# Performance work log

Measured on AMD Instinct MI355X. Metric: run time of the kernel, lower is better.

## Reference

```python
import jax, jax.numpy as jnp
import numpy as np

N_NODES = 50000
VOCAB = 2048
HID = 256
N_EDGES = 1600000


def setup_inputs() -> dict:
    key = jax.random.key(0)
    ks = jax.random.split(key, 7)
    context = jax.random.normal(ks[0], (N_NODES, VOCAB), dtype=jnp.float32)
    adj_row = jax.random.randint(ks[1], (N_EDGES,), 0, N_NODES, dtype=jnp.int64)
    adj_col = jax.random.randint(ks[2], (N_EDGES,), 0, N_NODES, dtype=jnp.int64)
    adj_val = jax.random.uniform(ks[3], (N_EDGES,), dtype=jnp.float32)
    # learned params
    context_weight = jax.random.normal(ks[4], (HID, VOCAB), dtype=jnp.float32) * 0.02
    out_w = jax.random.normal(ks[5], (VOCAB, HID), dtype=jnp.float32) * 0.02
    out_b = jnp.zeros((VOCAB,), dtype=jnp.float32)
    return {
        "context": context,
        "adj_row": adj_row,
        "adj_col": adj_col,
        "adj_val": adj_val,
        "context_weight": context_weight,
        "out_w": out_w,
        "out_b": out_b,
    }


def reference(context, adj_row, adj_col, adj_val, context_weight, out_w, out_b):
    # support = context @ context_weight.T : [N, hid]
    support = jnp.einsum('nv,hv->nh', context, context_weight)
    # spmm: out[r] += val * support[c]  (COO sparse-dense matmul)
    gathered = support[adj_col] * adj_val[:, None]          # [E, hid]
    agg = jax.ops.segment_sum(gathered, adj_row, num_segments=N_NODES)  # [N, hid]
    score = jax.nn.relu(agg)
    # out linear: hid -> vocab
    output = jnp.einsum('nh,vh->nv', score, out_w) + out_b  # [N, vocab]
    return output
```

## Files before the change

kernel.cpp:

```cpp
#include <hip/hip_runtime.h>
#include <hip/hip_bf16.h>

#define N_NODES 50000
#define VOCAB   2048
#define HID     256
#define N_EDGES 1600000

typedef __attribute__((ext_vector_type(8))) __bf16 bf16x8;
typedef __attribute__((ext_vector_type(4))) __bf16 bf16x4;
typedef __attribute__((ext_vector_type(4))) float  f32x4;

__device__ __forceinline__ void gl_lds16(const void* g, void* l) {
    __builtin_amdgcn_global_load_lds(
        (const __attribute__((address_space(1))) void*)g,
        (__attribute__((address_space(3))) void*)l, 16, 0, 0);
}

#define ZERO_NB 49
__global__ __launch_bounds__(256) void phase1(
    const float* __restrict__ w, __bf16* __restrict__ wb, int n4,
    int* __restrict__ cnt, int ncnt)
{
    int bid = blockIdx.x;
    if (bid < ZERO_NB) {
        const int base = bid * 1024 + threadIdx.x * 4;
        if (base + 3 < ncnt)      *(int4*)&cnt[base] = make_int4(0, 0, 0, 0);
        else                      for (int i = 0; i < 4; ++i)
                                      if (base + i < ncnt) cnt[base + i] = 0;
        return;
    }
    const int t = (bid - ZERO_NB) * 256 + threadIdx.x;
    if (t < n4) {
        const float4 v = ((const float4*)w)[t];
        bf16x4 p = { (__bf16)v.x, (__bf16)v.y, (__bf16)v.z, (__bf16)v.w };
        ((bf16x4*)wb)[t] = p;
    }
}

#define HIST_NB 96
#define CVTW_NB 64
__global__ __launch_bounds__(256) void phase2(
    const float*  __restrict__ Af,
    const __bf16* __restrict__ Bb,
    __bf16*       __restrict__ Cb,
    int M,
    const int*    __restrict__ arow, int* __restrict__ cnt, int E,
    const float*  __restrict__ w2,   __bf16* __restrict__ w2b, int n4w)
{
    const int tid = threadIdx.x;
    int bid = blockIdx.x;

    if (bid < HIST_NB) {
        const int stride = HIST_NB * 256;
        for (int e4 = bid * 256 + tid; e4 < E / 4; e4 += stride) {
            const int4 r = ((const int4*)arow)[e4];
            atomicAdd(&cnt[r.x], 1); atomicAdd(&cnt[r.y], 1);
            atomicAdd(&cnt[r.z], 1); atomicAdd(&cnt[r.w], 1);
        }
        return;
    }
    bid -= HIST_NB;
    if (bid < CVTW_NB) {
        const int stride = CVTW_NB * 256;
        for (int t = bid * 256 + tid; t < n4w; t += stride) {
            const float4 v = ((const float4*)w2)[t];
            bf16x4 p = { (__bf16)v.x, (__bf16)v.y, (__bf16)v.z, (__bf16)v.w };
            ((bf16x4*)w2b)[t] = p;
        }
        return;
    }
    bid -= CVTW_NB;

    constexpr int K = 2048, N = 256, BM = 64, BK = 32, nkt = K / BK;
    __shared__ float  sAf[3][BM * BK];
    __shared__ __bf16 sB [3][N  * BK];

    const int lane = tid & 63;
    const int wn   = tid >> 6;
    const int half = lane >> 4;
    const int r16  = lane & 15;
    const int m0   = bid * BM;

    f32x4 acc[4][4] = {};

    auto stage = [&](int kt, int b) {
        const int k0 = kt * BK;
        #pragma unroll
        for (int i = 0; i < 2; ++i) {
            const int s   = i * 256 + tid;
            const int row = s >> 3, c = s & 7;
            const int csw = c ^ (row & 7);
            int gr = m0 + row; if (gr >= M) gr = M - 1;
            gl_lds16(&Af[(size_t)gr * K + k0 + csw * 4], &sAf[b][s * 4]);
        }
        #pragma unroll
        for (int i = 0; i < 4; ++i) {
            const int s   = i * 256 + tid;
            const int row = s >> 2, c = s & 3;
            const int csw = c ^ (row & 3);
            gl_lds16(&Bb[(size_t)row * K + k0 + csw * 8], &sB[b][s * 8]);
        }
    };
    auto step = [&](int b) {
        bf16x8 bfr[4];
        #pragma unroll
        for (int n = 0; n < 4; ++n) {
            const int brow = wn * 64 + n * 16 + r16;
            bfr[n] = *(const bf16x8*)&sB[b][brow * 32 + (half ^ (brow & 3)) * 8];
        }
        #pragma unroll
        for (int m = 0; m < 4; ++m) {
            const int arw = m * 16 + r16;
            const int rx  = arw & 7;
            const f32x4 lo = *(const f32x4*)&sAf[b][arw * 32 + ((2 * half)     ^ rx) * 4];
            const f32x4 hi = *(const f32x4*)&sAf[b][arw * 32 + ((2 * half + 1) ^ rx) * 4];
            const bf16x8 af = { (__bf16)lo.x, (__bf16)lo.y, (__bf16)lo.z, (__bf16)lo.w,
                                (__bf16)hi.x, (__bf16)hi.y, (__bf16)hi.z, (__bf16)hi.w };
            #pragma unroll
            for (int n = 0; n < 4; ++n)
                acc[m][n] = __builtin_amdgcn_mfma_f32_16x16x32_bf16(
                                af, bfr[n], acc[m][n], 0, 0, 0);
        }
    };

    stage(0, 0);
    stage(1, 1);
    for (int t = 0; t < nkt; ++t) {
        if (t + 1 < nkt) asm volatile("s_waitcnt vmcnt(6)" ::: "memory");
        else             asm volatile("s_waitcnt vmcnt(0)" ::: "memory");
        __builtin_amdgcn_s_barrier();
        __builtin_amdgcn_sched_barrier(0);
        step(t % 3);
        if (t + 2 < nkt) stage(t + 2, (t + 2) % 3);
    }

    #pragma unroll
    for (int m = 0; m < 4; ++m) {
        #pragma unroll
        for (int j = 0; j < 4; ++j) {
            const int gr = m0 + m * 16 + half * 4 + j;
            if (gr >= M) continue;
            #pragma unroll
            for (int n = 0; n < 4; ++n) {
                const int gc = wn * 64 + n * 16 + r16;
                Cb[(size_t)gr * N + gc] = (__bf16)acc[m][n][j];
            }
        }
    }
}

#define SCAN_NB 49

__global__ __launch_bounds__(256) void scan1(
    const int* __restrict__ cnt, int* __restrict__ bsum, int n)
{
    __shared__ int red[256];
    const int base = blockIdx.x * 1024 + threadIdx.x * 4;
    int s = 0;
    #pragma unroll
    for (int i = 0; i < 4; ++i) { const int idx = base + i; if (idx < n) s += cnt[idx]; }
    red[threadIdx.x] = s;
    __syncthreads();
    for (int off = 128; off > 0; off >>= 1) {
        if (threadIdx.x < off) red[threadIdx.x] += red[threadIdx.x + off];
        __syncthreads();
    }
    if (threadIdx.x == 0) bsum[blockIdx.x] = red[0];
}

__global__ __launch_bounds__(256) void scan3m(
    const int* __restrict__ cnt, const int* __restrict__ bsum,
    int* __restrict__ ptr, int* __restrict__ cursor, int n, int E)
{
    __shared__ int hs[256];
    __shared__ int pre[256];
    const int tid = threadIdx.x;
    pre[tid] = (tid < blockIdx.x && tid < SCAN_NB) ? bsum[tid] : 0;
    __syncthreads();
    for (int off = 128; off > 0; off >>= 1) {
        if (tid < off) pre[tid] += pre[tid + off];
        __syncthreads();
    }
    const int bbase = pre[0];

    const int base = blockIdx.x * 1024 + tid * 4;
    int loc[4]; int s = 0;
    #pragma unroll
    for (int i = 0; i < 4; ++i) {
        const int idx = base + i;
        loc[i] = (idx < n) ? cnt[idx] : 0;
        s += loc[i];
    }
    hs[tid] = s;
    __syncthreads();
    for (int off = 1; off < 256; off <<= 1) {
        int v = (tid >= off) ? hs[tid - off] : 0;
        __syncthreads();
        hs[tid] += v;
        __syncthreads();
    }
    int run = bbase + ((tid == 0) ? 0 : hs[tid - 1]);
    #pragma unroll
    for (int i = 0; i < 4; ++i) {
        const int idx = base + i;
        if (idx < n) { ptr[idx] = run; cursor[idx] = run; }
        run += loc[i];
    }
    if (blockIdx.x == 0 && tid == 0) ptr[n] = E;
}

__global__ __launch_bounds__(256) void csr_fill(
    const int*   __restrict__ arow,
    const int*   __restrict__ acol,
    const float* __restrict__ aval,
    int*         __restrict__ cursor,
    int2*        __restrict__ cpair,
    int E)
{
    const int stride = gridDim.x * blockDim.x;
    for (int e4 = blockIdx.x * blockDim.x + threadIdx.x; e4 < E / 4; e4 += stride) {
        const int4   r = ((const int4*)arow)[e4];
        const int4   c = ((const int4*)acol)[e4];
        const float4 v = ((const float4*)aval)[e4];
        int p;
        p = atomicAdd(&cursor[r.x], 1); cpair[p] = make_int2(c.x, __float_as_int(v.x));
        p = atomicAdd(&cursor[r.y], 1); cpair[p] = make_int2(c.y, __float_as_int(v.y));
        p = atomicAdd(&cursor[r.z], 1); cpair[p] = make_int2(c.z, __float_as_int(v.z));
        p = atomicAdd(&cursor[r.w], 1); cpair[p] = make_int2(c.w, __float_as_int(v.w));
    }
}

__global__ __launch_bounds__(256) void spmm_gather(
    const int*    __restrict__ ptr,
    const int2*   __restrict__ cpair,
    const __bf16* __restrict__ support,
    __bf16*       __restrict__ agg,
    int n)
{
    const int tid  = threadIdx.x;
    const int lane = tid & 63;
    const int row  = blockIdx.x * 4 + (tid >> 6);
    if (row >= n) return;
    const int l32 = lane & 31, ep = lane >> 5;
    const int beg = ptr[row], end = ptr[row + 1];

    float a[8] = {0.f, 0.f, 0.f, 0.f, 0.f, 0.f, 0.f, 0.f};

    auto fma8 = [&](float v, const uint4& s) {
        a[0] += v * __uint_as_float(s.x << 16);
        a[1] += v * __uint_as_float(s.x & 0xFFFF0000u);
        a[2] += v * __uint_as_float(s.y << 16);
        a[3] += v * __uint_as_float(s.y & 0xFFFF0000u);
        a[4] += v * __uint_as_float(s.z << 16);
        a[5] += v * __uint_as_float(s.z & 0xFFFF0000u);
        a[6] += v * __uint_as_float(s.w << 16);
        a[7] += v * __uint_as_float(s.w & 0xFFFF0000u);
    };

    int i = beg;
    for (; i + 16 <= end; i += 16) {
        int2 p[8];
        #pragma unroll
        for (int u = 0; u < 8; ++u) p[u] = cpair[i + 2 * u + ep];
        uint4 s[8];
        #pragma unroll
        for (int u = 0; u < 8; ++u)
            s[u] = *(const uint4*)&support[(size_t)p[u].x * HID + l32 * 8];
        #pragma unroll
        for (int u = 0; u < 8; ++u) fma8(__int_as_float(p[u].y), s[u]);
    }
    for (; i + 2 <= end; i += 2) {
        const int2 p = cpair[i + ep];
        const uint4 s = *(const uint4*)&support[(size_t)p.x * HID + l32 * 8];
        fma8(__int_as_float(p.y), s);
    }
    if (i < end && ep == 0) {
        const int2 p = cpair[i];
        const uint4 s = *(const uint4*)&support[(size_t)p.x * HID + l32 * 8];
        fma8(__int_as_float(p.y), s);
    }

    #pragma unroll
    for (int k = 0; k < 8; ++k) a[k] += __shfl_xor(a[k], 32);

    if (ep == 0) {
        bf16x8 o = { (__bf16)fmaxf(a[0], 0.f), (__bf16)fmaxf(a[1], 0.f),
                     (__bf16)fmaxf(a[2], 0.f), (__bf16)fmaxf(a[3], 0.f),
                     (__bf16)fmaxf(a[4], 0.f), (__bf16)fmaxf(a[5], 0.f),
                     (__bf16)fmaxf(a[6], 0.f), (__bf16)fmaxf(a[7], 0.f) };
        *(bf16x8*)&agg[(size_t)row * HID + l32 * 8] = o;
    }
}

__global__ __launch_bounds__(256) void gemm2(
    const __bf16* __restrict__ Ab,
    const __bf16* __restrict__ Bb,
    const float*  __restrict__ bias,
    float*        __restrict__ C,
    int M)
{
    constexpr int K = 256, N = 2048, BM = 128, BN = 128, BK = 32;
    constexpr int NBY = N / BN, nkt = K / BK;
    __shared__ __bf16 sA[3][BM * BK];
    __shared__ __bf16 sB[3][BN * BK];

    const int tid  = threadIdx.x;
    const int lane = tid & 63;
    const int wid  = tid >> 6;
    const int wm   = wid >> 1;
    const int wn   = wid & 1;
    const int half = lane >> 4;
    const int r16  = lane & 15;

    const int nwg = gridDim.x, cpx = nwg >> 3;
    const int wg  = (blockIdx.x & 7) * cpx + (blockIdx.x >> 3);
    const int m0  = (wg / NBY) * BM;
    const int n0  = (wg % NBY) * BN;

    f32x4 acc[4][4] = {};

    auto stage = [&](int kt, int b) {
        const int k0 = kt * BK;
        #pragma unroll
        for (int i = 0; i < 2; ++i) {
            const int s   = i * 256 + tid;
            const int row = s >> 2, c = s & 3;
            const int csw = c ^ (row & 3);
            int gr = m0 + row; if (gr >= M) gr = M - 1;
            gl_lds16(&Ab[(size_t)gr * K + k0 + csw * 8], &sA[b][s * 8]);
        }
        #pragma unroll
        for (int i = 0; i < 2; ++i) {
            const int s   = i * 256 + tid;
            const int row = s >> 2, c = s & 3;
            const int csw = c ^ (row & 3);
            gl_lds16(&Bb[(size_t)(n0 + row) * K + k0 + csw * 8], &sB[b][s * 8]);
        }
    };
    auto step = [&](int b) {
        bf16x8 bfr[4];
        #pragma unroll
        for (int n = 0; n < 4; ++n) {
            const int brow = wn * 64 + n * 16 + r16;
            bfr[n] = *(const bf16x8*)&sB[b][brow * 32 + (half ^ (brow & 3)) * 8];
        }
        #pragma unroll
        for (int m = 0; m < 4; ++m) {
            const int arw = wm * 64 + m * 16 + r16;
            const bf16x8 af = *(const bf16x8*)&sA[b][arw * 32 + (half ^ (arw & 3)) * 8];
            #pragma unroll
            for (int n = 0; n < 4; ++n)
                acc[m][n] = __builtin_amdgcn_mfma_f32_16x16x32_bf16(
                                af, bfr[n], acc[m][n], 0, 0, 0);
        }
    };

    stage(0, 0);
    stage(1, 1);
    for (int t = 0; t < nkt; ++t) {
        if (t + 1 < nkt) asm volatile("s_waitcnt vmcnt(4)" ::: "memory");
        else             asm volatile("s_waitcnt vmcnt(0)" ::: "memory");
        __builtin_amdgcn_s_barrier();
        __builtin_amdgcn_sched_barrier(0);
        step(t % 3);
        if (t + 2 < nkt) stage(t + 2, (t + 2) % 3);
    }

    #pragma unroll
    for (int m = 0; m < 4; ++m) {
        #pragma unroll
        for (int j = 0; j < 4; ++j) {
            const int gr = m0 + wm * 64 + m * 16 + half * 4 + j;
            if (gr >= M) continue;
            #pragma unroll
            for (int n = 0; n < 4; ++n) {
                const int gc = n0 + wn * 64 + n * 16 + r16;
                __builtin_nontemporal_store(acc[m][n][j] + bias[gc],
                                            &C[(size_t)gr * N + gc]);
            }
        }
    }
}

extern "C" void kernel_launch(void* const* d_in, const int* in_sizes, int n_in,
                              void* d_out, int out_size, void* d_ws, size_t ws_size,
                              hipStream_t stream) {
    const float* context  = (const float*)d_in[0];
    const int*   adj_row  = (const int*)  d_in[1];
    const int*   adj_col  = (const int*)  d_in[2];
    const float* adj_val  = (const float*)d_in[3];
    const float* ctx_w    = (const float*)d_in[4];
    const float* out_w    = (const float*)d_in[5];
    const float* out_b    = (const float*)d_in[6];
    float*       out      = (float*)d_out;

    char* ws = (char*)d_ws;
    __bf16* support_b = (__bf16*)ws;  ws += (size_t)N_NODES * HID * 2;
    __bf16* agg_b     = (__bf16*)ws;  ws += (size_t)N_NODES * HID * 2;
    __bf16* ctxw_b    = (__bf16*)ws;  ws += (size_t)HID * VOCAB * 2;
    __bf16* outw_b    = (__bf16*)ws;  ws += (size_t)VOCAB * HID * 2;
    int*    csr_ptr   = (int*)ws;     ws += ((size_t)N_NODES + 16) * 4;
    int*    cnt       = (int*)ws;     ws += (size_t)N_NODES * 4;
    int*    cursor    = (int*)ws;     ws += (size_t)N_NODES * 4;
    int*    bsum      = (int*)ws;     ws += 320;
    int2*   cpair     = (int2*)ws;    ws += (size_t)N_EDGES * 8;

    constexpr int N4 = HID * VOCAB / 4;

    phase1<<<dim3(ZERO_NB + (N4 + 255) / 256), 256, 0, stream>>>(
        ctx_w, ctxw_b, N4, cnt, N_NODES);

    phase2<<<dim3(HIST_NB + CVTW_NB + (N_NODES + 63) / 64), 256, 0, stream>>>(
        context, ctxw_b, support_b, N_NODES,
        adj_row, cnt, N_EDGES,
        out_w, outw_b, N4);

    scan1<<<SCAN_NB, 256, 0, stream>>>(cnt, bsum, N_NODES);
    scan3m<<<SCAN_NB, 256, 0, stream>>>(cnt, bsum, csr_ptr, cursor, N_NODES, N_EDGES);

    csr_fill<<<512, 256, 0, stream>>>(
        adj_row, adj_col, adj_val, cursor, cpair, N_EDGES);

    spmm_gather<<<(N_NODES + 3) / 4, 256, 0, stream>>>(
        csr_ptr, cpair, support_b, agg_b, N_NODES);

    gemm2<<<dim3(((N_NODES + 127) / 128) * (VOCAB / 128)), 256, 0, stream>>>(
        agg_b, outw_b, out_b, out, N_NODES);
}
```

Baseline: 494.1 us.

## Pipeline SpMM row chunks with output GEMM tiles across fused launches

Splits the rows into three chunks and fuses the SpMM gather for chunk i+1 with the output GEMM for chunk i in one launch, so the gather-bound and MFMA-bound blocks share the GPU at the same time. This is meant to hide the SpMM latency and fill the tail of each phase. In exchange it adds launches, and the mixed kernels carry the GEMM's shared-memory footprint for SpMM blocks too, which may lower occupancy for the gather work.

After: 558.1 us. 13.0% more time.

```diff
diff --git a/kernel.cpp b/kernel.cpp
--- a/kernel.cpp
+++ b/kernel.cpp
@@ -230,17 +230,17 @@
     }
 }
 
-__global__ __launch_bounds__(256) void spmm_gather(
+__device__ __forceinline__ void spmm_rows(
+    int bid, int tid,
     const int*    __restrict__ ptr,
     const int2*   __restrict__ cpair,
     const __bf16* __restrict__ support,
     __bf16*       __restrict__ agg,
-    int n)
-{
-    const int tid  = threadIdx.x;
+    int rowLo, int rowHi)
+{
     const int lane = tid & 63;
-    const int row  = blockIdx.x * 4 + (tid >> 6);
-    if (row >= n) return;
+    const int row  = rowLo + bid * 4 + (tid >> 6);
+    if (row >= rowHi) return;
     const int l32 = lane & 31, ep = lane >> 5;
     const int beg = ptr[row], end = ptr[row + 1];
 
@@ -292,19 +292,19 @@
     }
 }
 
-__global__ __launch_bounds__(256) void gemm2(
+__device__ __forceinline__ void gemm2_tile(
+    int bid, int nBlocks, int tid,
     const __bf16* __restrict__ Ab,
     const __bf16* __restrict__ Bb,
     const float*  __restrict__ bias,
     float*        __restrict__ C,
-    int M)
+    int M, int tLo)
 {
     constexpr int K = 256, N = 2048, BM = 128, BN = 128, BK = 32;
     constexpr int NBY = N / BN, nkt = K / BK;
     __shared__ __bf16 sA[3][BM * BK];
     __shared__ __bf16 sB[3][BN * BK];
 
-    const int tid  = threadIdx.x;
     const int lane = tid & 63;
     const int wid  = tid >> 6;
     const int wm   = wid >> 1;
@@ -312,9 +312,9 @@
     const int half = lane >> 4;
     const int r16  = lane & 15;
 
-    const int nwg = gridDim.x, cpx = nwg >> 3;
-    const int wg  = (blockIdx.x & 7) * cpx + (blockIdx.x >> 3);
-    const int m0  = (wg / NBY) * BM;
+    const int cpx = nBlocks >> 3;
+    const int wg  = (bid & 7) * cpx + (bid >> 3);
+    const int m0  = (tLo + wg / NBY) * BM;
     const int n0  = (wg % NBY) * BN;
 
     f32x4 acc[4][4] = {};
@@ -380,6 +380,38 @@
             }
         }
     }
+}
+
+__global__ __launch_bounds__(256) void spmm_k(
+    const int* __restrict__ ptr, const int2* __restrict__ cpair,
+    const __bf16* __restrict__ support, __bf16* __restrict__ agg,
+    int rowLo, int rowHi)
+{
+    spmm_rows(blockIdx.x, threadIdx.x, ptr, cpair, support, agg, rowLo, rowHi);
+}
+
+__global__ __launch_bounds__(256) void gemm2_k(
+    const __bf16* __restrict__ Ab, const __bf16* __restrict__ Bb,
+    const float* __restrict__ bias, float* __restrict__ C,
+    int M, int tLo)
+{
+    gemm2_tile(blockIdx.x, gridDim.x, threadIdx.x, Ab, Bb, bias, C, M, tLo);
+}
+
+__global__ __launch_bounds__(256) void spmm_gemm2_k(
+    const int* __restrict__ ptr, const int2* __restrict__ cpair,
+    const __bf16* __restrict__ support, __bf16* __restrict__ agg,
+    int rowLo, int rowHi, int spmmNB,
+    const __bf16* __restrict__ Ab, const __bf16* __restrict__ Bb,
+    const float* __restrict__ bias, float* __restrict__ C,
+    int M, int tLo, int g2NB)
+{
+    const int bid = blockIdx.x;
+    if (bid < spmmNB) {
+        spmm_rows(bid, threadIdx.x, ptr, cpair, support, agg, rowLo, rowHi);
+        return;
+    }
+    gemm2_tile(bid - spmmNB, g2NB, threadIdx.x, Ab, Bb, bias, C, M, tLo);
 }
 
 extern "C" void kernel_launch(void* const* d_in, const int* in_sizes, int n_in,
@@ -421,9 +453,21 @@
     csr_fill<<<512, 256, 0, stream>>>(
         adj_row, adj_col, adj_val, cursor, cpair, N_EDGES);
 
-    spmm_gather<<<(N_NODES + 3) / 4, 256, 0, stream>>>(
-        csr_ptr, cpair, support_b, agg_b, N_NODES);
-
-    gemm2<<<dim3(((N_NODES + 127) / 128) * (VOCAB / 128)), 256, 0, stream>>>(
-        agg_b, outw_b, out_b, out, N_NODES);
-}
+    constexpr int T0 = 130, T1 = 130, T2 = 131;
+    constexpr int R1 = T0 * 128;
+    constexpr int R2 = (T0 + T1) * 128;
+    constexpr int S0 = (R1 + 3) / 4;
+    constexpr int S1 = (R2 - R1 + 3) / 4;
+    constexpr int S2 = (N_NODES - R2 + 3) / 4;
+    constexpr int G0 = T0 * 16, G1 = T1 * 16, G2 = T2 * 16;
+
+    spmm_k<<<S0, 256, 0, stream>>>(csr_ptr, cpair, support_b, agg_b, 0, R1);
+    spmm_gemm2_k<<<S1 + G0, 256, 0, stream>>>(
+        csr_ptr, cpair, support_b, agg_b, R1, R2, S1,
+        agg_b, outw_b, out_b, out, N_NODES, 0, G0);
+    spmm_gemm2_k<<<S2 + G1, 256, 0, stream>>>(
+        csr_ptr, cpair, support_b, agg_b, R2, N_NODES, S2,
+        agg_b, outw_b, out_b, out, N_NODES, T0, G1);
+    gemm2_k<<<G2, 256, 0, stream>>>(
+        agg_b, outw_b, out_b, out, N_NODES, T0 + T1);
+}
```

## Load GEMM1 B operand directly to registers and enlarge K tile with double buffering

Applied to the files above, without the earlier changes.

The first GEMM (context × weightᵀ) no longer stages the bf16 weight tile through LDS. Each wave now reads its B fragments straight from global memory into registers. The K tile grows from 32 to 128, and the A tile moves from triple-buffered to double-buffered LDS with a wider swizzle. The aim is to cut LDS traffic and barrier count per K step. The cost is a full vmcnt(0) wait each iteration, so prefetch depth is lower, and B loads from global may be less coalesced and add latency.

Result: no change. 491.1 us (median of 2 runs) (-0.6%).

```diff
diff --git a/kernel.cpp b/kernel.cpp
--- a/kernel.cpp
+++ b/kernel.cpp
@@ -71,9 +71,8 @@
     }
     bid -= CVTW_NB;
 
-    constexpr int K = 2048, N = 256, BM = 64, BK = 32, nkt = K / BK;
-    __shared__ float  sAf[3][BM * BK];
-    __shared__ __bf16 sB [3][N  * BK];
+    constexpr int K = 2048, N = 256, BM = 64, BK = 128, nkt = K / BK;
+    __shared__ float sAf[2][BM * BK];
 
     const int lane = tid & 63;
     const int wn   = tid >> 6;
@@ -86,52 +85,51 @@
     auto stage = [&](int kt, int b) {
         const int k0 = kt * BK;
         #pragma unroll
-        for (int i = 0; i < 2; ++i) {
+        for (int i = 0; i < 8; ++i) {
             const int s   = i * 256 + tid;
-            const int row = s >> 3, c = s & 7;
-            const int csw = c ^ (row & 7);
+            const int row = s >> 5, c = s & 31;
+            const int csw = (c & 24) | ((c & 7) ^ (row & 7));
             int gr = m0 + row; if (gr >= M) gr = M - 1;
-            gl_lds16(&Af[(size_t)gr * K + k0 + csw * 4], &sAf[b][s * 4]);
-        }
-        #pragma unroll
-        for (int i = 0; i < 4; ++i) {
-            const int s   = i * 256 + tid;
-            const int row = s >> 2, c = s & 3;
-            const int csw = c ^ (row & 3);
-            gl_lds16(&Bb[(size_t)row * K + k0 + csw * 8], &sB[b][s * 8]);
+            gl_lds16(&Af[(size_t)gr * K + k0 + csw * 4], &sAf[b][row * BK + c * 4]);
         }
     };
-    auto step = [&](int b) {
-        bf16x8 bfr[4];
-        #pragma unroll
-        for (int n = 0; n < 4; ++n) {
-            const int brow = wn * 64 + n * 16 + r16;
-            bfr[n] = *(const bf16x8*)&sB[b][brow * 32 + (half ^ (brow & 3)) * 8];
-        }
-        #pragma unroll
-        for (int m = 0; m < 4; ++m) {
-            const int arw = m * 16 + r16;
-            const int rx  = arw & 7;
-            const f32x4 lo = *(const f32x4*)&sAf[b][arw * 32 + ((2 * half)     ^ rx) * 4];
-            const f32x4 hi = *(const f32x4*)&sAf[b][arw * 32 + ((2 * half + 1) ^ rx) * 4];
-            const bf16x8 af = { (__bf16)lo.x, (__bf16)lo.y, (__bf16)lo.z, (__bf16)lo.w,
-                                (__bf16)hi.x, (__bf16)hi.y, (__bf16)hi.z, (__bf16)hi.w };
+
+    stage(0, 0);
+    for (int t = 0; t < nkt; ++t) {
+        const int cur = t & 1;
+        asm volatile("s_waitcnt vmcnt(0)" ::: "memory");
+        __builtin_amdgcn_s_barrier();
+        __builtin_amdgcn_sched_barrier(0);
+
+        const int k0 = t * BK;
+        uint4 bq[4][4];
+        #pragma unroll
+        for (int sub = 0; sub < 4; ++sub)
             #pragma unroll
             for (int n = 0; n < 4; ++n)
-                acc[m][n] = __builtin_amdgcn_mfma_f32_16x16x32_bf16(
-                                af, bfr[n], acc[m][n], 0, 0, 0);
-        }
-    };
-
-    stage(0, 0);
-    stage(1, 1);
-    for (int t = 0; t < nkt; ++t) {
-        if (t + 1 < nkt) asm volatile("s_waitcnt vmcnt(6)" ::: "memory");
-        else             asm volatile("s_waitcnt vmcnt(0)" ::: "memory");
-        __builtin_amdgcn_s_barrier();
+                bq[sub][n] = *(const uint4*)&Bb[
+                    (size_t)(wn * 64 + n * 16 + r16) * K + k0 + sub * 32 + half * 8];
         __builtin_amdgcn_sched_barrier(0);
-        step(t % 3);
-        if (t + 2 < nkt) stage(t + 2, (t + 2) % 3);
+
+        if (t + 1 < nkt) stage(t + 1, cur ^ 1);
+
+        #pragma unroll
+        for (int sub = 0; sub < 4; ++sub) {
+            const int cb = sub * 8;
+            #pragma unroll
+            for (int m = 0; m < 4; ++m) {
+                const int arw = m * 16 + r16;
+                const int rx  = arw & 7;
+                const f32x4 lo = *(const f32x4*)&sAf[cur][arw * BK + (cb + ((2 * half)     ^ rx)) * 4];
+                const f32x4 hi = *(const f32x4*)&sAf[cur][arw * BK + (cb + ((2 * half + 1) ^ rx)) * 4];
+                const bf16x8 af = { (__bf16)lo.x, (__bf16)lo.y, (__bf16)lo.z, (__bf16)lo.w,
+                                    (__bf16)hi.x, (__bf16)hi.y, (__bf16)hi.z, (__bf16)hi.w };
+                #pragma unroll
+                for (int n = 0; n < 4; ++n)
+                    acc[m][n] = __builtin_amdgcn_mfma_f32_16x16x32_bf16(
+                                    af, *(const bf16x8*)&bq[sub][n], acc[m][n], 0, 0, 0);
+            }
+        }
     }
 
     #pragma unroll
@@ -410,7 +408,7 @@
     phase1<<<dim3(ZERO_NB + (N4 + 255) / 256), 256, 0, stream>>>(
         ctx_w, ctxw_b, N4, cnt, N_NODES);
 
-    phase2<<<dim3(HIST_NB + CVTW_NB + (N_NODES + 63) / 64), 256, 0, stream>>>(
+    phase2<<<dim3(HIST_NB + CVTW_NB + (N_NODES + 63) / 64), dim3(256), 0, stream>>>(
         context, ctxw_b, support_b, N_NODES,
         adj_row, cnt, N_EDGES,
         out_w, outw_b, N4);
```
